# Kernel optimization log

Measured on AMD Instinct MI355X. Metric: run time of the kernel, lower is better.

Reference implementation:

```python
import jax, jax.numpy as jnp
import numpy as np

D = 1024; H = 16; N = 64; F = 4096
B = 1; T = 2048
W_LORA = 64; A_LORA = 64; V_LORA = 32; G_LORA = 128


def rmsnorm(x, w, eps=1e-6):
    x32 = x.astype(jnp.float32)
    var = jnp.mean(x32 * x32, axis=-1, keepdims=True)
    return w * (x32 * jax.lax.rsqrt(var + eps))


def rwkv7_scan(r, w_log, k, v, a, b, state):
    # r,w_log,k,v,a,b: [B,T,H,N]; state: [B,H,N,N] (value dim, key dim)
    decay = jnp.exp(w_log)  # kernel applies exp to the log-decay w = -exp(w_pre)
    def step(S, inp):
        r_t, d_t, k_t, v_t, a_t, b_t = inp  # each [B,H,N]
        sa = jnp.einsum('bhij,bhj->bhi', S, a_t)
        S = S * d_t[:, :, None, :] + sa[..., None] * b_t[:, :, None, :] + v_t[..., None] * k_t[:, :, None, :]
        o_t = jnp.einsum('bhij,bhj->bhi', S, r_t)
        return S, o_t
    seq = tuple(jnp.moveaxis(t, 1, 0) for t in (r, decay, k, v, a, b))  # [T,B,H,N]
    state_f, o = jax.lax.scan(step, state, seq)
    return jnp.moveaxis(o, 0, 1), state_f  # [B,T,H,N], [B,H,N,N]


def setup_inputs() -> dict:
    key = jax.random.key(0)
    ks = iter(jax.random.split(key, 64))
    def nrm(shape, s=1.0):
        return jax.random.normal(next(ks), shape, dtype=jnp.float32) * s
    def uni(shape):
        return jax.random.uniform(next(ks), shape, dtype=jnp.float32)
    WS = 0.02  # weight scale for big matrices
    inp = {
        'x': nrm((B, T, D)),
        'x_prev': nrm((B, D)),
        'v_first': nrm((B, T, D)),
        'state': jnp.zeros((B, H, N, N), jnp.float32),
        'ln1_w': jnp.ones((D,), jnp.float32),
        'ln2_w': jnp.ones((D,), jnp.float32),
        'x_r': uni((1, 1, D)), 'x_w': uni((1, 1, D)), 'x_k': uni((1, 1, D)),
        'x_v': uni((1, 1, D)), 'x_a': uni((1, 1, D)), 'x_g': uni((1, 1, D)),
        'w0': nrm((1, 1, D), 0.5), 'w1': nrm((D, W_LORA), WS), 'w2': nrm((W_LORA, D), WS),
        'a0': nrm((1, 1, D), 0.1), 'a1': nrm((D, A_LORA), WS), 'a2': nrm((A_LORA, D), WS),
        'v0': nrm((1, 1, D), 0.1), 'v1': nrm((D, V_LORA), WS), 'v2': nrm((V_LORA, D), WS),
        'g1': nrm((D, G_LORA), WS), 'g2': nrm((G_LORA, D), WS),
        'k_k': uni((D,)), 'k_a': uni((D,)), 'r_k': nrm((D,), 0.1),
        'R_': nrm((D, D), WS), 'K_': nrm((D, D), WS), 'V_': nrm((D, D), WS), 'O_': nrm((D, D), WS),
        'gate_w': nrm((D, F), WS), 'up_w': nrm((D, F), WS), 'down_w': nrm((F, D), WS),
    }
    return inp


def _block(x, x_prev, v_first, state, ln1_w, ln2_w, x_r, x_w, x_k, x_v, x_a, x_g,
           w0, w1, w2, a0, a1, a2, v0, v1, v2, g1, g2, k_k, k_a, r_k,
           R_, K_, V_, O_, gate_w, up_w, down_w):
    Bx, Tx, _ = x.shape
    xn = rmsnorm(x, ln1_w)  # ln1
    # token shift
    xx = jnp.concatenate([x_prev[:, None, :], xn[:, :-1]], axis=1) - xn
    xr = xn + xx * x_r; xw = xn + xx * x_w; xk = xn + xx * x_k
    xv = xn + xx * x_v; xa = xn + xx * x_a; xg = xn + xx * x_g
    r = xr @ R_
    w_pre = -jax.nn.softplus(-(w0 + jnp.tanh(xw @ w1) @ w2)) - 0.5
    k = xk @ K_
    v = xv @ V_
    a = jax.nn.sigmoid(a0 + (xa @ a1) @ a2)
    g = jax.nn.sigmoid(xg @ g1) @ g2
    kk = (k * k_k).reshape(Bx, Tx, H, N)
    kk = kk / jnp.maximum(jnp.linalg.norm(kk, axis=-1, keepdims=True), 1e-12)
    kk = kk.reshape(Bx, Tx, H * N)
    k = k * (1 + (a - 1) * k_a)
    # layer_id > 0: lerp toward v_first
    v = v + (v_first - v) * jax.nn.sigmoid(v0 + (xv @ v1) @ v2)
    w_log = -jnp.exp(w_pre)  # log-decay passed to the recurrent kernel
    aa = -kk
    bb = kk * a
    hv = lambda t: t.reshape(Bx, Tx, H, N)
    o, state_f = rwkv7_scan(hv(r), hv(w_log), hv(k), hv(v), hv(aa), hv(bb), state)
    o = o.reshape(Bx, Tx, H * N)
    bonus = ((r * k * r_k).reshape(Bx, Tx, H, N).sum(-1, keepdims=True) * v.reshape(Bx, Tx, H, N)).reshape(Bx, Tx, H * N)
    o = o + bonus
    x = x + (o * g) @ O_
    # SwiGLU MLP
    xm = rmsnorm(x, ln2_w)
    x = x + (jax.nn.silu(xm @ gate_w) * (xm @ up_w)) @ down_w
    return x, xn[:, -1], state_f


def reference(x, x_prev, v_first, state, ln1_w, ln2_w, x_r, x_w, x_k, x_v, x_a, x_g,
              w0, w1, w2, a0, a1, a2, v0, v1, v2, g1, g2, k_k, k_a, r_k,
              R_, K_, V_, O_, gate_w, up_w, down_w):
    return _block(x, x_prev, v_first, state, ln1_w, ln2_w, x_r, x_w, x_k, x_v, x_a, x_g,
                  w0, w1, w2, a0, a1, a2, v0, v1, v2, g1, g2, k_k, k_a, r_k,
                  R_, K_, V_, O_, gate_w, up_w, down_w)
```

## Files before the change

kernel.cpp:

```cpp
#include <hip/hip_runtime.h>
#include <math.h>

#define T_ 2048
#define D_ 1024
#define H_ 16
#define N_ 64
#define F_ 4096
#define NCHUNK 64
#define CLEN 32

typedef __attribute__((ext_vector_type(8))) short bf16x8;
typedef __attribute__((ext_vector_type(4))) float f32x4;
typedef __attribute__((address_space(3))) unsigned int lds_u32_t;
typedef __attribute__((address_space(1))) const unsigned int glb_u32_t;

static __device__ __forceinline__ float sigf(float x) { return 1.0f / (1.0f + __expf(-x)); }

static __device__ __forceinline__ ushort f2bf(float f) {
    union { float f; unsigned u; } c; c.f = f;
    unsigned r = (c.u + 0x7FFFu + ((c.u >> 16) & 1u)) >> 16;
    return (ushort)r;
}
static __device__ __forceinline__ float bf2f(ushort h) {
    union { unsigned u; float f; } c; c.u = ((unsigned)h) << 16;
    return c.f;
}

static __device__ __forceinline__ void st4(float* p, float4 v) { *(float4*)p = v; }
static __device__ __forceinline__ void st4(ushort* p, float4 v) {
    ushort4 o; o.x = f2bf(v.x); o.y = f2bf(v.y); o.z = f2bf(v.z); o.w = f2bf(v.w);
    *(ushort4*)p = o;
}

template <typename OutT>
__global__ __launch_bounds__(256) void rmsnorm_kernel(const float* __restrict__ x,
                                                      const float* __restrict__ w,
                                                      OutT* __restrict__ out,
                                                      float* __restrict__ last) {
    const int t = blockIdx.x;
    const int tid = threadIdx.x;
    const float4* xr = (const float4*)(x + (size_t)t * D_);
    float4 v = xr[tid];
    float ss = v.x * v.x + v.y * v.y + v.z * v.z + v.w * v.w;
    ss += __shfl_xor(ss, 1);
    ss += __shfl_xor(ss, 2);
    ss += __shfl_xor(ss, 4);
    ss += __shfl_xor(ss, 8);
    ss += __shfl_xor(ss, 16);
    ss += __shfl_xor(ss, 32);
    __shared__ float red[4];
    if ((tid & 63) == 0) red[tid >> 6] = ss;
    __syncthreads();
    float tot = red[0] + red[1] + red[2] + red[3];
    float scale = rsqrtf(tot * (1.0f / (float)D_) + 1e-6f);
    float4 wv = ((const float4*)w)[tid];
    float4 o;
    o.x = wv.x * v.x * scale;
    o.y = wv.y * v.y * scale;
    o.z = wv.z * v.z * scale;
    o.w = wv.w * v.w * scale;
    st4(out + (size_t)t * D_ + tid * 4, o);
    if (last != nullptr && t == T_ - 1) ((float4*)last)[tid] = o;
}

__global__ __launch_bounds__(256) void rmsnorm_reduce2(
    const float* __restrict__ x, const float* __restrict__ p0, const float* __restrict__ p1,
    const float* __restrict__ w, float* __restrict__ resid_out, ushort* __restrict__ xm) {
    const int t = blockIdx.x;
    const int tid = threadIdx.x;
    const size_t base = (size_t)t * D_ + tid * 4;
    float4 v = *(const float4*)(x + base);
    float4 a = *(const float4*)(p0 + base);
    float4 b = *(const float4*)(p1 + base);
    v.x += a.x + b.x; v.y += a.y + b.y; v.z += a.z + b.z; v.w += a.w + b.w;
    st4(resid_out + base, v);
    float ss = v.x * v.x + v.y * v.y + v.z * v.z + v.w * v.w;
    ss += __shfl_xor(ss, 1);
    ss += __shfl_xor(ss, 2);
    ss += __shfl_xor(ss, 4);
    ss += __shfl_xor(ss, 8);
    ss += __shfl_xor(ss, 16);
    ss += __shfl_xor(ss, 32);
    __shared__ float red[4];
    if ((tid & 63) == 0) red[tid >> 6] = ss;
    __syncthreads();
    float tot = red[0] + red[1] + red[2] + red[3];
    float scale = rsqrtf(tot * (1.0f / (float)D_) + 1e-6f);
    float4 wv = ((const float4*)w)[tid];
    float4 o;
    o.x = wv.x * v.x * scale;
    o.y = wv.y * v.y * scale;
    o.z = wv.z * v.z * scale;
    o.w = wv.w * v.w * scale;
    st4(xm + base, o);
}

__global__ __launch_bounds__(256) void add4_kernel(float* __restrict__ out,
                                                   const float* __restrict__ p,
                                                   int n4slice) {
    const int i = blockIdx.x * 256 + threadIdx.x;
    const float4* p4 = (const float4*)p;
    float4 o = ((const float4*)out)[i];
    float4 a = p4[i], b = p4[i + n4slice], c = p4[i + 2 * n4slice], d = p4[i + 3 * n4slice];
    o.x += (a.x + b.x) + (c.x + d.x);
    o.y += (a.y + b.y) + (c.y + d.y);
    o.z += (a.z + b.z) + (c.z + d.z);
    o.w += (a.w + b.w) + (c.w + d.w);
    ((float4*)out)[i] = o;
}

__global__ __launch_bounds__(256) void shift_kernel(
    const float* __restrict__ xn, const float* __restrict__ x_prev,
    const float* __restrict__ cr, const float* __restrict__ cw, const float* __restrict__ ck,
    const float* __restrict__ cv, const float* __restrict__ ca, const float* __restrict__ cg,
    ushort* __restrict__ xr, ushort* __restrict__ xw, ushort* __restrict__ xk,
    ushort* __restrict__ xv, ushort* __restrict__ xa, ushort* __restrict__ xg) {
    const int i = blockIdx.x * 256 + threadIdx.x;
    const int t = i >> 8, j = i & 255;
    const float4* xn4 = (const float4*)xn;
    float4 cur = xn4[i];
    float4 prev = (t == 0) ? ((const float4*)x_prev)[j] : xn4[i - 256];
    float4 xx;
    xx.x = prev.x - cur.x;
    xx.y = prev.y - cur.y;
    xx.z = prev.z - cur.z;
    xx.w = prev.w - cur.w;
#define APPLY(dst, c)                                   \
    {                                                   \
        float4 cc = ((const float4*)c)[j];              \
        float4 o;                                       \
        o.x = cur.x + xx.x * cc.x;                      \
        o.y = cur.y + xx.y * cc.y;                      \
        o.z = cur.z + xx.z * cc.z;                      \
        o.w = cur.w + xx.w * cc.w;                      \
        st4(dst + (size_t)i * 4, o);                    \
    }
    APPLY(xr, cr)
    APPLY(xw, cw)
    APPLY(xk, ck)
    APPLY(xv, cv)
    APPLY(xa, ca)
    APPLY(xg, cg)
#undef APPLY
}

struct TDesc { const float* in; ushort* out; int K, N, off; };
struct TPack { TDesc d[15]; };

__global__ __launch_bounds__(256) void transpose_cast_multi(TPack p) {
    __shared__ float tile[32][33];
    const int bid = blockIdx.x;
    int di = 0;
#pragma unroll
    for (int i = 1; i < 15; i++)
        if (bid >= p.d[i].off) di = i;
    const TDesc d = p.d[di];
    const int local = bid - d.off;
    const int nt = d.N >> 5;
    const int bx = local % nt, by = local / nt;
    const int tx = threadIdx.x & 31, ty = threadIdx.x >> 5;
    const int n0 = bx * 32, k0 = by * 32;
#pragma unroll
    for (int i = 0; i < 4; i++)
        tile[ty + i * 8][tx] = d.in[(size_t)(k0 + ty + i * 8) * d.N + n0 + tx];
    __syncthreads();
#pragma unroll
    for (int i = 0; i < 4; i++)
        d.out[(size_t)(n0 + ty + i * 8) * d.K + k0 + tx] = f2bf(tile[tx][ty + i * 8]);
}

template <typename OutT, bool PARTIAL>
__global__ __launch_bounds__(256) void mfma_gemm(
    const ushort* __restrict__ A, const ushort* __restrict__ BT, OutT* __restrict__ C,
    const float* res, int M, int Ntot, int K, int klen, int epi) {
    __shared__ ushort As[2][128 * 32];
    __shared__ ushort Bs[2][128 * 32];
    const int tid = threadIdx.x;
    const int wave = tid >> 6, lane = tid & 63;
    const int wr = wave >> 1, wc = wave & 1;
    const int lrow = lane & 15, quad = lane >> 4;
    int bx = blockIdx.x, by = blockIdx.y;
    if (gridDim.x == 8 && gridDim.y == 16) {
        const int bid = by * 8 + bx;
        const int k = bid & 7, i = bid >> 3;
        bx = ((k & 1) << 2) + (i & 3);
        by = ((k >> 1) << 2) + (i >> 2);
    }
    const int m0 = by * 128, n0 = bx * 128;
    const int kbase = blockIdx.z * klen;
    const int srow = lane >> 2;
    const int scol = (lane & 3) << 3;

    f32x4 acc[4][4] = {};

    auto stage = [&](int buf, int kk) {
#pragma unroll
        for (int j = 0; j < 2; j++) {
            const int chunk = 2 * wave + j;
            const ushort* ga = A + (size_t)(m0 + chunk * 16 + srow) * K + kk + scol;
            __builtin_amdgcn_global_load_lds((glb_u32_t*)ga,
                                             (lds_u32_t*)&As[buf][chunk * 512], 16, 0, 0);
            const int brow = n0 + chunk * 16 + srow;
            if (brow < Ntot) {
                const ushort* gb = BT + (size_t)brow * K + kk + scol;
                __builtin_amdgcn_global_load_lds((glb_u32_t*)gb,
                                                 (lds_u32_t*)&Bs[buf][chunk * 512], 16, 0, 0);
            }
        }
    };

    stage(0, kbase);
    __syncthreads();
    int cur = 0;
    for (int k0 = kbase; k0 < kbase + klen; k0 += 32) {
        if (k0 + 32 < kbase + klen) stage(cur ^ 1, k0 + 32);
        bf16x8 af[4], bfr[4];
#pragma unroll
        for (int mi = 0; mi < 4; mi++)
            af[mi] = *(const bf16x8*)&As[cur][(wr * 64 + mi * 16 + lrow) * 32 + quad * 8];
#pragma unroll
        for (int ni = 0; ni < 4; ni++)
            bfr[ni] = *(const bf16x8*)&Bs[cur][(wc * 64 + ni * 16 + lrow) * 32 + quad * 8];
#pragma unroll
        for (int mi = 0; mi < 4; mi++)
#pragma unroll
            for (int ni = 0; ni < 4; ni++)
                acc[mi][ni] = __builtin_amdgcn_mfma_f32_16x16x32_bf16(af[mi], bfr[ni], acc[mi][ni], 0, 0, 0);
        __syncthreads();
        cur ^= 1;
    }

    const size_t zoff = PARTIAL ? (size_t)blockIdx.z * M * Ntot : 0;
#pragma unroll
    for (int mi = 0; mi < 4; mi++) {
#pragma unroll
        for (int r = 0; r < 4; r++) {
            const int row = m0 + wr * 64 + mi * 16 + quad * 4 + r;
#pragma unroll
            for (int ni = 0; ni < 4; ni++) {
                const int col = n0 + wc * 64 + ni * 16 + lrow;
                if (col < Ntot) {
                    const size_t idx = (size_t)row * Ntot + col;
                    float val = acc[mi][ni][r];
                    if constexpr (PARTIAL) {
                        ((float*)C)[idx + zoff] = val;
                    } else {
                        if (epi == 1) val += res[idx];
                        if constexpr (sizeof(OutT) == 2) C[idx] = (OutT)f2bf(val);
                        else C[idx] = (OutT)val;
                    }
                }
            }
        }
    }
}

struct MMDesc {
    const ushort* A; const ushort* BT;
    float* Cf; ushort* Cb;
    const float* res; const float* res2; const float* bias;
    int Ntot, K, epi;
};
template <int NZ>
struct MMPack { MMDesc d[NZ]; };

template <int NZ>
__global__ __launch_bounds__(256) void mfma_gemm_multi(MMPack<NZ> p) {
    const MMDesc d = p.d[blockIdx.z];
    const int n0 = blockIdx.x * 128;
    if (n0 >= d.Ntot) return;
    __shared__ ushort As[2][128 * 32];
    __shared__ ushort Bs[2][128 * 32];
    const int tid = threadIdx.x;
    const int wave = tid >> 6, lane = tid & 63;
    const int wr = wave >> 1, wc = wave & 1;
    const int lrow = lane & 15, quad = lane >> 4;
    const int m0 = blockIdx.y * 128;
    const int srow = lane >> 2;
    const int scol = (lane & 3) << 3;
    const int K = d.K, Ntot = d.Ntot;

    f32x4 acc[4][4] = {};

    auto stage = [&](int buf, int kk) {
#pragma unroll
        for (int j = 0; j < 2; j++) {
            const int chunk = 2 * wave + j;
            const ushort* ga = d.A + (size_t)(m0 + chunk * 16 + srow) * K + kk + scol;
            __builtin_amdgcn_global_load_lds((glb_u32_t*)ga,
                                             (lds_u32_t*)&As[buf][chunk * 512], 16, 0, 0);
            const int brow = n0 + chunk * 16 + srow;
            if (brow < Ntot) {
                const ushort* gb = d.BT + (size_t)brow * K + kk + scol;
                __builtin_amdgcn_global_load_lds((glb_u32_t*)gb,
                                                 (lds_u32_t*)&Bs[buf][chunk * 512], 16, 0, 0);
            }
        }
    };

    stage(0, 0);
    __syncthreads();
    int cur = 0;
    for (int k0 = 0; k0 < K; k0 += 32) {
        if (k0 + 32 < K) stage(cur ^ 1, k0 + 32);
        bf16x8 af[4], bfr[4];
#pragma unroll
        for (int mi = 0; mi < 4; mi++)
            af[mi] = *(const bf16x8*)&As[cur][(wr * 64 + mi * 16 + lrow) * 32 + quad * 8];
#pragma unroll
        for (int ni = 0; ni < 4; ni++)
            bfr[ni] = *(const bf16x8*)&Bs[cur][(wc * 64 + ni * 16 + lrow) * 32 + quad * 8];
#pragma unroll
        for (int mi = 0; mi < 4; mi++)
#pragma unroll
            for (int ni = 0; ni < 4; ni++)
                acc[mi][ni] = __builtin_amdgcn_mfma_f32_16x16x32_bf16(af[mi], bfr[ni], acc[mi][ni], 0, 0, 0);
        __syncthreads();
        cur ^= 1;
    }

#pragma unroll
    for (int mi = 0; mi < 4; mi++) {
#pragma unroll
        for (int r = 0; r < 4; r++) {
            const int row = m0 + wr * 64 + mi * 16 + quad * 4 + r;
#pragma unroll
            for (int ni = 0; ni < 4; ni++) {
                const int col = n0 + wc * 64 + ni * 16 + lrow;
                if (col < Ntot) {
                    const size_t idx = (size_t)row * Ntot + col;
                    float val = acc[mi][ni][r];
                    switch (d.epi) {
                        case 3: val = tanhf(val); break;
                        case 4: val = sigf(val); break;
                        case 5: val = sigf(d.bias[col] + val); break;
                        case 6: val = __expf(-0.60653065971263342f * sigf(d.bias[col] + val)); break;
                        case 7: {
                            float vr = d.res[idx];
                            val = vr + (d.res2[idx] - vr) * sigf(d.bias[col] + val);
                        } break;
                        default: break;
                    }
                    if (d.Cb) d.Cb[idx] = f2bf(val);
                    else d.Cf[idx] = val;
                }
            }
        }
    }
}

__global__ __launch_bounds__(256) void kk_kernel(float* __restrict__ k,
                                                 const float* __restrict__ a_sig,
                                                 const float* __restrict__ k_k,
                                                 const float* __restrict__ k_a,
                                                 float* __restrict__ kk,
                                                 float* __restrict__ mb) {
    const int b = blockIdx.x * 4 + (threadIdx.x >> 6);
    const int t = b >> 4, h = b & 15;
    const int lane = threadIdx.x & 63;
    const size_t idx = (size_t)t * D_ + h * N_ + lane;
    const int wi = h * N_ + lane;
    const float kraw = k[idx];
    const float kv = kraw * k_k[wi];
    float ss = kv * kv;
    ss += __shfl_xor(ss, 1);
    ss += __shfl_xor(ss, 2);
    ss += __shfl_xor(ss, 4);
    ss += __shfl_xor(ss, 8);
    ss += __shfl_xor(ss, 16);
    ss += __shfl_xor(ss, 32);
    const float nrm = fmaxf(sqrtf(ss), 1e-12f);
    const float kkn = kv / nrm;
    kk[idx] = kkn;
    mb[idx] = -kkn * a_sig[idx];
    k[idx] = kraw * (1.0f + (a_sig[idx] - 1.0f) * k_a[wi]);
}

#define FOR16(M) M(0) M(1) M(2) M(3) M(4) M(5) M(6) M(7) \
                 M(8) M(9) M(10) M(11) M(12) M(13) M(14) M(15)

__global__ __launch_bounds__(64, 1) void scan_pass1(
    const float* __restrict__ gR, const float* __restrict__ gD, const float* __restrict__ gK,
    const float* __restrict__ gV, const float* __restrict__ gKK, const float* __restrict__ gMB,
    float* __restrict__ Pbuf, float* __restrict__ Lbuf,
    float* __restrict__ zbuf, float* __restrict__ olbuf) {
    const int bid = blockIdx.x;
    const int h = bid & 15;
    const int c = bid >> 4;
    const int lane = threadIdx.x;
    const int hb = h * N_;
    const int t0 = c * CLEN;
    const int tend = t0 + CLEN - 1;

    __shared__ __align__(16) unsigned char ring[2 * 2048];

    const int rsel = lane >> 4;
    const int sub4 = (lane & 15) << 2;
    const float* p1 = (rsel == 0 ? gR : rsel == 1 ? gD : rsel == 2 ? gK : gKK)
                      + (size_t)t0 * D_ + hb + sub4;
    const float* p2 = (rsel == 1 ? gV : gMB) + (size_t)t0 * D_ + hb + sub4;

#define DECLP(q) f32x4 sp##q = {(lane == 4 * q + 0) ? 1.0f : 0.0f, \
                                (lane == 4 * q + 1) ? 1.0f : 0.0f, \
                                (lane == 4 * q + 2) ? 1.0f : 0.0f, \
                                (lane == 4 * q + 3) ? 1.0f : 0.0f};
    FOR16(DECLP)
#undef DECLP
#define DECLL(q) f32x4 sl##q = {0.f, 0.f, 0.f, 0.f};
    FOR16(DECLL)
#undef DECLL

    float4 r0a, r0b, r1a, r1b, r2a, r2b, r3a, r3b;

#define LOADQ(qa, qb, tt) {                                                  \
        const size_t _adv = (size_t)((tt) - t0) * D_;                        \
        qa = *(const float4*)(p1 + _adv);                                    \
        qb = *(const float4*)(p2 + _adv); }
#define WRITEQ(sl, qa, qb) {                                                 \
        *(float4*)(ring + (sl) * 2048 + lane * 16) = qa;                     \
        *(float4*)(ring + (sl) * 2048 + 1024 + lane * 16) = qb; }
#define PA(q) { const f32x4 kk4 = sKKr[q];                                   \
        pacc += sp##q * kk4; lacc += sl##q * kk4; }
#define PB(q) {                                                   \
        const f32x4 d4 = sDr[q];                                  \
        const f32x4 k4 = sKr[q];                                  \
        const f32x4 m4 = sMBr[q];                                 \
        const f32x4 r4 = sRr[q];                                  \
        sp##q = sp##q * d4 + m4 * sapP;                           \
        sl##q = sl##q * d4 + (m4 * sapL + k4 * vv);               \
        oP += sp##q * r4;                                         \
        oL += sl##q * r4;                                         \
    }
#define COMPUTE(sl, tt) {                                                    \
        const unsigned char* sb = (const unsigned char*)ring + (sl) * 2048;  \
        const f32x4* sRr = (const f32x4*)(sb);                               \
        const f32x4* sDr = (const f32x4*)(sb + 256);                         \
        const f32x4* sKr = (const f32x4*)(sb + 512);                         \
        const f32x4* sKKr = (const f32x4*)(sb + 768);                        \
        const f32x4* sMBr = (const f32x4*)(sb + 1024);                       \
        const float* sVr = (const float*)(sb + 1280);                        \
        f32x4 pacc = {0.f, 0.f, 0.f, 0.f};                                   \
        f32x4 lacc = {0.f, 0.f, 0.f, 0.f};                                   \
        FOR16(PA)                                                            \
        const float sapP = (pacc.x + pacc.y) + (pacc.z + pacc.w);            \
        const float sapL = (lacc.x + lacc.y) + (lacc.z + lacc.w);            \
        const float vv = sVr[lane];                                          \
        f32x4 oP = {0.f, 0.f, 0.f, 0.f};                                     \
        f32x4 oL = {0.f, 0.f, 0.f, 0.f};                                     \
        FOR16(PB)                                                            \
        zbuf[(size_t)(tt) * D_ + hb + lane] = (oP.x + oP.y) + (oP.z + oP.w); \
        olbuf[(size_t)(tt) * D_ + hb + lane] = (oL.x + oL.y) + (oL.z + oL.w); }

    LOADQ(r0a, r0b, t0)
    LOADQ(r1a, r1b, t0 + 1)
    LOADQ(r2a, r2b, t0 + 2)
    LOADQ(r3a, r3b, t0 + 3)
    WRITEQ(0, r0a, r0b)

    for (int t = t0; t < t0 + CLEN; t += 4) {
        WRITEQ(1, r1a, r1b)
        LOADQ(r0a, r0b, (t + 4 > tend ? tend : t + 4))
        COMPUTE(0, t)
        WRITEQ(0, r2a, r2b)
        LOADQ(r1a, r1b, (t + 5 > tend ? tend : t + 5))
        COMPUTE(1, t + 1)
        WRITEQ(1, r3a, r3b)
        LOADQ(r2a, r2b, (t + 6 > tend ? tend : t + 6))
        COMPUTE(0, t + 2)
        WRITEQ(0, r0a, r0b)
        LOADQ(r3a, r3b, (t + 7 > tend ? tend : t + 7))
        COMPUTE(1, t + 3)
    }
#undef COMPUTE
#undef PB
#undef PA
#undef WRITEQ
#undef LOADQ

    const size_t base = ((size_t)c * 16 + h) * 4096 + (size_t)lane * 64;
#define STP(q) *(f32x4*)(Pbuf + base + 4 * q) = sp##q;
    FOR16(STP)
#undef STP
#define STL(q) *(f32x4*)(Lbuf + base + 4 * q) = sl##q;
    FOR16(STL)
#undef STL
}

__global__ __launch_bounds__(256) void scan_combine(
    const float* __restrict__ state_in, const float* __restrict__ Pbuf,
    const float* __restrict__ Lbuf, float* __restrict__ SstT, float* __restrict__ state_out) {
    const int h = blockIdx.x >> 2, rg = blockIdx.x & 3;
    const int tid = threadIdx.x;
    const int i = tid >> 4, j4 = (tid & 15) << 2;
    const int gi = rg * 16 + i;
    __shared__ float Sl[16][68];
    __shared__ float Pl[64][68];

    float4 sv = *(const float4*)(state_in + (size_t)h * 4096 + gi * 64 + j4);
    *(float4*)&Sl[i][j4] = sv;
    __syncthreads();

    for (int c = 0; c < NCHUNK; c++) {
        const size_t cb = ((size_t)c * 16 + h) * 4096;
        float4 scur = *(const float4*)&Sl[i][j4];
        SstT[cb + (size_t)(j4 + 0) * 64 + gi] = scur.x;
        SstT[cb + (size_t)(j4 + 1) * 64 + gi] = scur.y;
        SstT[cb + (size_t)(j4 + 2) * 64 + gi] = scur.z;
        SstT[cb + (size_t)(j4 + 3) * 64 + gi] = scur.w;
#pragma unroll
        for (int q = 0; q < 4; q++) {
            const int pr = (tid >> 4) + q * 16;
            *(float4*)&Pl[pr][j4] = *(const float4*)(Pbuf + cb + (size_t)pr * 64 + j4);
        }
        __syncthreads();
        float4 acc = *(const float4*)(Lbuf + cb + (size_t)gi * 64 + j4);
#pragma unroll 8
        for (int m = 0; m < 64; m++) {
            const float smv = Sl[i][m];
            const float4 p4 = *(const float4*)&Pl[m][j4];
            acc.x = fmaf(smv, p4.x, acc.x);
            acc.y = fmaf(smv, p4.y, acc.y);
            acc.z = fmaf(smv, p4.z, acc.z);
            acc.w = fmaf(smv, p4.w, acc.w);
        }
        __syncthreads();
        *(float4*)&Sl[i][j4] = acc;
        __syncthreads();
    }
    *(float4*)(state_out + (size_t)h * 4096 + gi * 64 + j4) = *(const float4*)&Sl[i][j4];
}

__global__ __launch_bounds__(256) void scan_fix(
    const float* __restrict__ zbuf, const float* __restrict__ olbuf,
    const float* __restrict__ SstT, float* __restrict__ o) {
    const int tg = blockIdx.x >> 4, h = blockIdx.x & 15;
    const int hb = h * N_;
    const int tid = threadIdx.x;
    const int tok = tid >> 4, i4 = (tid & 15) << 2;
    const int tbase = tg * 16;
    const int c = tbase / CLEN;
    __shared__ float zl[16][68];
    __shared__ float Sl[64][68];

    *(float4*)&zl[tok][i4] = *(const float4*)(zbuf + (size_t)(tbase + tok) * D_ + hb + i4);
    const size_t cb = ((size_t)c * 16 + h) * 4096;
#pragma unroll
    for (int q = 0; q < 4; q++) {
        const int jr = (tid >> 4) + q * 16;
        *(float4*)&Sl[jr][i4] = *(const float4*)(SstT + cb + (size_t)jr * 64 + i4);
    }
    __syncthreads();
    float4 acc = *(const float4*)(olbuf + (size_t)(tbase + tok) * D_ + hb + i4);
#pragma unroll 8
    for (int j = 0; j < 64; j++) {
        const float zv = zl[tok][j];
        const float4 p4 = *(const float4*)&Sl[j][i4];
        acc.x = fmaf(zv, p4.x, acc.x);
        acc.y = fmaf(zv, p4.y, acc.y);
        acc.z = fmaf(zv, p4.z, acc.z);
        acc.w = fmaf(zv, p4.w, acc.w);
    }
    *(float4*)(o + (size_t)(tbase + tok) * D_ + hb + i4) = acc;
}

__global__ __launch_bounds__(256) void bonus_kernel(const float* __restrict__ o,
                                                    const float* __restrict__ r,
                                                    const float* __restrict__ k,
                                                    const float* __restrict__ v,
                                                    const float* __restrict__ g,
                                                    const float* __restrict__ r_k,
                                                    ushort* __restrict__ og) {
    const int b = blockIdx.x * 4 + (threadIdx.x >> 6);
    const int t = b >> 4, h = b & 15;
    const int lane = threadIdx.x & 63;
    const size_t idx = (size_t)t * D_ + h * N_ + lane;
    float c = r[idx] * k[idx] * r_k[h * N_ + lane];
    c += __shfl_xor(c, 1);
    c += __shfl_xor(c, 2);
    c += __shfl_xor(c, 4);
    c += __shfl_xor(c, 8);
    c += __shfl_xor(c, 16);
    c += __shfl_xor(c, 32);
    const float on = o[idx] + c * v[idx];
    og[idx] = f2bf(on * g[idx]);
}

__global__ __launch_bounds__(256) void mulz_kernel(const ushort* __restrict__ Z,
                                                   ushort* __restrict__ Hb) {
    const int idx = blockIdx.x * 256 + threadIdx.x;
    const int t = idx >> 10;
    const int j = (idx & 1023) << 2;
    const ushort4 zg = *(const ushort4*)(Z + (size_t)t * 8192 + j);
    const ushort4 zu = *(const ushort4*)(Z + (size_t)t * 8192 + 4096 + j);
    ushort4 o;
    float g0 = bf2f(zg.x), g1 = bf2f(zg.y), g2 = bf2f(zg.z), g3 = bf2f(zg.w);
    o.x = f2bf(g0 * sigf(g0) * bf2f(zu.x));
    o.y = f2bf(g1 * sigf(g1) * bf2f(zu.y));
    o.z = f2bf(g2 * sigf(g2) * bf2f(zu.z));
    o.w = f2bf(g3 * sigf(g3) * bf2f(zu.w));
    *(ushort4*)(Hb + (size_t)t * 4096 + j) = o;
}

extern "C" void kernel_launch(void* const* d_in, const int* in_sizes, int n_in,
                              void* d_out, int out_size, void* d_ws, size_t ws_size,
                              hipStream_t stream) {
    const float* x      = (const float*)d_in[0];
    const float* x_prev = (const float*)d_in[1];
    const float* v_first= (const float*)d_in[2];
    const float* state  = (const float*)d_in[3];
    const float* ln1_w  = (const float*)d_in[4];
    const float* ln2_w  = (const float*)d_in[5];
    const float* x_r    = (const float*)d_in[6];
    const float* x_w    = (const float*)d_in[7];
    const float* x_k    = (const float*)d_in[8];
    const float* x_v    = (const float*)d_in[9];
    const float* x_a    = (const float*)d_in[10];
    const float* x_g    = (const float*)d_in[11];
    const float* w0     = (const float*)d_in[12];
    const float* w1     = (const float*)d_in[13];
    const float* w2     = (const float*)d_in[14];
    const float* a0     = (const float*)d_in[15];
    const float* a1     = (const float*)d_in[16];
    const float* a2     = (const float*)d_in[17];
    const float* v0     = (const float*)d_in[18];
    const float* v1     = (const float*)d_in[19];
    const float* v2     = (const float*)d_in[20];
    const float* g1     = (const float*)d_in[21];
    const float* g2     = (const float*)d_in[22];
    const float* k_k    = (const float*)d_in[23];
    const float* k_a    = (const float*)d_in[24];
    const float* r_k    = (const float*)d_in[25];
    const float* R_     = (const float*)d_in[26];
    const float* K_     = (const float*)d_in[27];
    const float* V_     = (const float*)d_in[28];
    const float* O_     = (const float*)d_in[29];
    const float* gate_w = (const float*)d_in[30];
    const float* up_w   = (const float*)d_in[31];
    const float* down_w = (const float*)d_in[32];

    float* ws = (float*)d_ws;
    const size_t U = (size_t)T_ * D_;
    float* u_r  = ws;
    float* u_k  = ws + 1 * U;
    float* u_v  = ws + 2 * U;
    float* u_dc = ws + 3 * U;
    float* u_kk = ws + 4 * U;
    float* u_mb = ws + 5 * U;
    float* u_g  = ws + 6 * U;
    float* u_ao = ws + 7 * U;
    ushort* XB = (ushort*)(ws + 8 * U);
    const size_t TD = U;
    ushort* XR = XB + 0 * TD;
    ushort* XW = XB + 1 * TD;
    ushort* XK = XB + 2 * TD;
    ushort* XV = XB + 3 * TD;
    ushort* XA = XB + 4 * TD;
    ushort* XG = XB + 5 * TD;
    float* Pbuf  = (float*)XB;
    float* Lbuf  = u_g;
    float* zbuf  = ws + 10 * U;
    float* olbuf = (float*)d_out;
    float* SstT  = u_dc;
    float* obuf  = u_mb;
    ushort* OG   = XB;
    ushort* XM   = (ushort*)(ws + 10 * U);
    float* Opart = ws + 4 * U;
    ushort* Zbuf = (ushort*)ws;
    ushort* Hbuf = (ushort*)(ws + 4 * U);
    float* Dpart = ws;
    ushort* WT = (ushort*)(ws + 11 * U);
    const size_t DD = (size_t)D_ * D_;
    const size_t DF = (size_t)D_ * F_;
    ushort* WTR = WT;
    ushort* WTK = WTR + DD;
    ushort* WTV = WTK + DD;
    ushort* WTO = WTV + DD;
    ushort* WTG = WTO + DD;
    ushort* WTU = WTG + DF;
    ushort* WTD = WTU + DF;
    ushort* WTw1 = WTD + DF;
    ushort* WTw2 = WTw1 + 64 * 1024;
    ushort* WTa1 = WTw2 + 64 * 1024;
    ushort* WTa2 = WTa1 + 64 * 1024;
    ushort* WTv1 = WTa2 + 64 * 1024;
    ushort* WTv2 = WTv1 + 32 * 1024;
    ushort* WTg1 = WTv2 + 32 * 1024;
    ushort* WTg2 = WTg1 + 128 * 1024;
    ushort* Lw = WTg2 + 128 * 1024;
    ushort* La = Lw + (size_t)T_ * 64;
    ushort* Lv = La + (size_t)T_ * 64;
    ushort* Lg = Lv + (size_t)T_ * 32;

    float* out_x = (float*)d_out;
    float* out_xn_last = out_x + (size_t)T_ * D_;
    float* out_state = out_xn_last + D_;

    TPack tp;
    int toff = 0, ti = 0;
    auto addT = [&](const float* in, ushort* out, int K, int N) {
        tp.d[ti].in = in; tp.d[ti].out = out; tp.d[ti].K = K; tp.d[ti].N = N; tp.d[ti].off = toff;
        toff += (N / 32) * (K / 32); ++ti;
    };
    addT(R_, WTR, D_, D_);
    addT(K_, WTK, D_, D_);
    addT(V_, WTV, D_, D_);
    addT(O_, WTO, D_, D_);
    addT(gate_w, WTG, D_, F_);
    addT(up_w, WTU, D_, F_);
    addT(down_w, WTD, F_, D_);
    addT(w1, WTw1, D_, 64);
    addT(w2, WTw2, 64, D_);
    addT(a1, WTa1, D_, 64);
    addT(a2, WTa2, 64, D_);
    addT(v1, WTv1, D_, 32);
    addT(v2, WTv2, 32, D_);
    addT(g1, WTg1, D_, 128);
    addT(g2, WTg2, 128, D_);
    transpose_cast_multi<<<toff, 256, 0, stream>>>(tp);

    rmsnorm_kernel<float><<<T_, 256, 0, stream>>>(x, ln1_w, out_x, out_xn_last);
    shift_kernel<<<T_, 256, 0, stream>>>(out_x, x_prev, x_r, x_w, x_k, x_v, x_a, x_g,
                                         XR, XW, XK, XV, XA, XG);
    auto mkmm = [](const ushort* A, const ushort* BT, float* Cf, ushort* Cb,
                   const float* res, const float* res2, const float* bias,
                   int Ntot, int K, int epi) {
        MMDesc m{A, BT, Cf, Cb, res, res2, bias, Ntot, K, epi};
        return m;
    };
    MMPack<7> pa;
    pa.d[0] = mkmm(XR, WTR, u_r, nullptr, nullptr, nullptr, nullptr, D_, D_, 0);
    pa.d[1] = mkmm(XK, WTK, u_k, nullptr, nullptr, nullptr, nullptr, D_, D_, 0);
    pa.d[2] = mkmm(XV, WTV, u_v, nullptr, nullptr, nullptr, nullptr, D_, D_, 0);
    pa.d[3] = mkmm(XW, WTw1, nullptr, Lw, nullptr, nullptr, nullptr, 64,  D_, 3);
    pa.d[4] = mkmm(XA, WTa1, nullptr, La, nullptr, nullptr, nullptr, 64,  D_, 0);
    pa.d[5] = mkmm(XV, WTv1, nullptr, Lv, nullptr, nullptr, nullptr, 32,  D_, 0);
    pa.d[6] = mkmm(XG, WTg1, nullptr, Lg, nullptr, nullptr, nullptr, 128, D_, 4);
    mfma_gemm_multi<7><<<dim3(8, 16, 7), 256, 0, stream>>>(pa);
    MMPack<3> pb;
    pb.d[0] = mkmm(Lw, WTw2, u_dc, nullptr, nullptr, nullptr, w0, D_, 64,  6);
    pb.d[1] = mkmm(La, WTa2, u_ao, nullptr, nullptr, nullptr, a0, D_, 64,  5);
    pb.d[2] = mkmm(Lv, WTv2, u_v,  nullptr, u_v, v_first,     v0, D_, 32,  7);
    mfma_gemm_multi<3><<<dim3(8, 16, 3), 256, 0, stream>>>(pb);
    kk_kernel<<<T_ * H_ / 4, 256, 0, stream>>>(u_k, u_ao, k_k, k_a, u_kk, u_mb);
    scan_pass1<<<NCHUNK * H_, 64, 0, stream>>>(u_r, u_dc, u_k, u_v, u_kk, u_mb,
                                               Pbuf, Lbuf, zbuf, olbuf);
    scan_combine<<<H_ * 4, 256, 0, stream>>>(state, Pbuf, Lbuf, SstT, out_state);
    mfma_gemm<float, false><<<dim3(8, 16), 256, 0, stream>>>(
        Lg, WTg2, u_g, nullptr, T_, D_, 128, 128, 0);
    scan_fix<<<(T_ / 16) * H_, 256, 0, stream>>>(zbuf, olbuf, SstT, obuf);
    bonus_kernel<<<T_ * H_ / 4, 256, 0, stream>>>(obuf, u_r, u_k, u_v, u_g, r_k, OG);
    mfma_gemm<float, true><<<dim3(8, 16, 2), 256, 0, stream>>>(
        OG, WTO, Opart, nullptr, T_, D_, D_, 512, 0);
    rmsnorm_reduce2<<<T_, 256, 0, stream>>>(x, Opart, Opart + U, ln2_w, out_x, XM);
    mfma_gemm<ushort, false><<<dim3(64, 16), 256, 0, stream>>>(
        XM, WTG, Zbuf, nullptr, T_, 2 * F_, D_, D_, 0);
    mulz_kernel<<<(T_ * (F_ / 4)) / 256, 256, 0, stream>>>(Zbuf, Hbuf);
    mfma_gemm<float, true><<<dim3(8, 16, 4), 256, 0, stream>>>(
        Hbuf, WTD, Dpart, nullptr, T_, D_, F_, 1024, 0);
    add4_kernel<<<(int)(U / 4 / 256), 256, 0, stream>>>(out_x, Dpart, (int)(U / 4));
}
```

Baseline: 647.8 us.

## Halve serial chunk-state combine via parallel pairwise merge and odd-chunk fill

```diff
diff --git a/kernel.cpp b/kernel.cpp
--- a/kernel.cpp
+++ b/kernel.cpp
@@ -486,6 +486,68 @@
 #undef STL
 }
 
+__global__ __launch_bounds__(64) void merge_pairs(float* __restrict__ Pbuf,
+                                                  float* __restrict__ Lbuf) {
+    const int h = blockIdx.x & 15, j = blockIdx.x >> 4;
+    const int t = threadIdx.x;
+    __shared__ float PaT[64][65];
+    __shared__ float LaT[64][65];
+    __shared__ float Pb[64][68];
+    const size_t ca = ((size_t)(2 * j) * 16 + h) * 4096;
+    const size_t cb = ((size_t)(2 * j + 1) * 16 + h) * 4096;
+#pragma unroll
+    for (int q = 0; q < 16; q++) {
+        const int idx = t + q * 64;
+        const int r = idx >> 4, c4 = (idx & 15) << 2;
+        float4 pa = *(const float4*)(Pbuf + ca + (size_t)r * 64 + c4);
+        float4 la = *(const float4*)(Lbuf + ca + (size_t)r * 64 + c4);
+        float4 pb = *(const float4*)(Pbuf + cb + (size_t)r * 64 + c4);
+        PaT[c4 + 0][r] = pa.x; PaT[c4 + 1][r] = pa.y;
+        PaT[c4 + 2][r] = pa.z; PaT[c4 + 3][r] = pa.w;
+        LaT[c4 + 0][r] = la.x; LaT[c4 + 1][r] = la.y;
+        LaT[c4 + 2][r] = la.z; LaT[c4 + 3][r] = la.w;
+        *(float4*)&Pb[r][c4] = pb;
+    }
+    __syncthreads();
+    const int cg = (t & 3) << 4;
+    const int r0 = (t >> 2) << 2;
+    float4 accP[4][4] = {};
+    float4 accL[4][4];
+#pragma unroll
+    for (int rr = 0; rr < 4; rr++)
+#pragma unroll
+        for (int e = 0; e < 4; e++)
+            accL[rr][e] = *(const float4*)(Lbuf + cb + (size_t)(r0 + rr) * 64 + cg + 4 * e);
+    for (int m = 0; m < 64; m++) {
+        float4 pb4[4];
+#pragma unroll
+        for (int e = 0; e < 4; e++) pb4[e] = *(const float4*)&Pb[m][cg + 4 * e];
+#pragma unroll
+        for (int rr = 0; rr < 4; rr++) {
+            const float pa = PaT[m][r0 + rr];
+            const float la = LaT[m][r0 + rr];
+#pragma unroll
+            for (int e = 0; e < 4; e++) {
+                accP[rr][e].x = fmaf(pa, pb4[e].x, accP[rr][e].x);
+                accP[rr][e].y = fmaf(pa, pb4[e].y, accP[rr][e].y);
+                accP[rr][e].z = fmaf(pa, pb4[e].z, accP[rr][e].z);
+                accP[rr][e].w = fmaf(pa, pb4[e].w, accP[rr][e].w);
+                accL[rr][e].x = fmaf(la, pb4[e].x, accL[rr][e].x);
+                accL[rr][e].y = fmaf(la, pb4[e].y, accL[rr][e].y);
+                accL[rr][e].z = fmaf(la, pb4[e].z, accL[rr][e].z);
+                accL[rr][e].w = fmaf(la, pb4[e].w, accL[rr][e].w);
+            }
+        }
+    }
+#pragma unroll
+    for (int rr = 0; rr < 4; rr++)
+#pragma unroll
+        for (int e = 0; e < 4; e++) {
+            *(float4*)(Pbuf + cb + (size_t)(r0 + rr) * 64 + cg + 4 * e) = accP[rr][e];
+            *(float4*)(Lbuf + cb + (size_t)(r0 + rr) * 64 + cg + 4 * e) = accL[rr][e];
+        }
+}
+
 __global__ __launch_bounds__(256) void scan_combine(
     const float* __restrict__ state_in, const float* __restrict__ Pbuf,
     const float* __restrict__ Lbuf, float* __restrict__ SstT, float* __restrict__ state_out) {
@@ -498,22 +560,39 @@
 
     float4 sv = *(const float4*)(state_in + (size_t)h * 4096 + gi * 64 + j4);
     *(float4*)&Sl[i][j4] = sv;
+
+    float4 rp0, rp1, rp2, rp3, rl;
+    {
+        const size_t cb = ((size_t)1 * 16 + h) * 4096;
+        rp0 = *(const float4*)(Pbuf + cb + (size_t)(i +  0) * 64 + j4);
+        rp1 = *(const float4*)(Pbuf + cb + (size_t)(i + 16) * 64 + j4);
+        rp2 = *(const float4*)(Pbuf + cb + (size_t)(i + 32) * 64 + j4);
+        rp3 = *(const float4*)(Pbuf + cb + (size_t)(i + 48) * 64 + j4);
+        rl  = *(const float4*)(Lbuf + cb + (size_t)gi * 64 + j4);
+    }
     __syncthreads();
 
-    for (int c = 0; c < NCHUNK; c++) {
-        const size_t cb = ((size_t)c * 16 + h) * 4096;
+    for (int c = 0; c < NCHUNK / 2; c++) {
+        *(float4*)&Pl[i +  0][j4] = rp0;
+        *(float4*)&Pl[i + 16][j4] = rp1;
+        *(float4*)&Pl[i + 32][j4] = rp2;
+        *(float4*)&Pl[i + 48][j4] = rp3;
+        float4 acc = rl;
+        const size_t so = ((size_t)(2 * c) * 16 + h) * 4096;
         float4 scur = *(const float4*)&Sl[i][j4];
-        SstT[cb + (size_t)(j4 + 0) * 64 + gi] = scur.x;
-        SstT[cb + (size_t)(j4 + 1) * 64 + gi] = scur.y;
-        SstT[cb + (size_t)(j4 + 2) * 64 + gi] = scur.z;
-        SstT[cb + (size_t)(j4 + 3) * 64 + gi] = scur.w;
-#pragma unroll
-        for (int q = 0; q < 4; q++) {
-            const int pr = (tid >> 4) + q * 16;
-            *(float4*)&Pl[pr][j4] = *(const float4*)(Pbuf + cb + (size_t)pr * 64 + j4);
+        SstT[so + (size_t)(j4 + 0) * 64 + gi] = scur.x;
+        SstT[so + (size_t)(j4 + 1) * 64 + gi] = scur.y;
+        SstT[so + (size_t)(j4 + 2) * 64 + gi] = scur.z;
+        SstT[so + (size_t)(j4 + 3) * 64 + gi] = scur.w;
+        __syncthreads();
+        if (c + 1 < NCHUNK / 2) {
+            const size_t cb = ((size_t)(2 * c + 3) * 16 + h) * 4096;
+            rp0 = *(const float4*)(Pbuf + cb + (size_t)(i +  0) * 64 + j4);
+            rp1 = *(const float4*)(Pbuf + cb + (size_t)(i + 16) * 64 + j4);
+            rp2 = *(const float4*)(Pbuf + cb + (size_t)(i + 32) * 64 + j4);
+            rp3 = *(const float4*)(Pbuf + cb + (size_t)(i + 48) * 64 + j4);
+            rl  = *(const float4*)(Lbuf + cb + (size_t)gi * 64 + j4);
         }
-        __syncthreads();
-        float4 acc = *(const float4*)(Lbuf + cb + (size_t)gi * 64 + j4);
 #pragma unroll 8
         for (int m = 0; m < 64; m++) {
             const float smv = Sl[i][m];
@@ -525,9 +604,50 @@
         }
         __syncthreads();
         *(float4*)&Sl[i][j4] = acc;
-        __syncthreads();
     }
     *(float4*)(state_out + (size_t)h * 4096 + gi * 64 + j4) = *(const float4*)&Sl[i][j4];
+}
+
+__global__ __launch_bounds__(256) void scan_oddfill(
+    const float* __restrict__ Pbuf, const float* __restrict__ Lbuf,
+    float* __restrict__ SstT) {
+    const int b = blockIdx.x;
+    const int rg = b & 3, h = (b >> 2) & 15, j = b >> 6;
+    const int tid = threadIdx.x;
+    const int i = tid >> 4, j4 = (tid & 15) << 2;
+    const int gi = rg * 16 + i;
+    __shared__ float Sl[16][68];
+    __shared__ float Pl[64][68];
+    const size_t ce = ((size_t)(2 * j) * 16 + h) * 4096;
+    const size_t co = ((size_t)(2 * j + 1) * 16 + h) * 4096;
+    {
+        float4 s;
+        s.x = SstT[ce + (size_t)(j4 + 0) * 64 + gi];
+        s.y = SstT[ce + (size_t)(j4 + 1) * 64 + gi];
+        s.z = SstT[ce + (size_t)(j4 + 2) * 64 + gi];
+        s.w = SstT[ce + (size_t)(j4 + 3) * 64 + gi];
+        *(float4*)&Sl[i][j4] = s;
+    }
+#pragma unroll
+    for (int q = 0; q < 4; q++) {
+        const int prq = i + q * 16;
+        *(float4*)&Pl[prq][j4] = *(const float4*)(Pbuf + ce + (size_t)prq * 64 + j4);
+    }
+    __syncthreads();
+    float4 acc = *(const float4*)(Lbuf + ce + (size_t)gi * 64 + j4);
+#pragma unroll 8
+    for (int m = 0; m < 64; m++) {
+        const float smv = Sl[i][m];
+        const float4 p4 = *(const float4*)&Pl[m][j4];
+        acc.x = fmaf(smv, p4.x, acc.x);
+        acc.y = fmaf(smv, p4.y, acc.y);
+        acc.z = fmaf(smv, p4.z, acc.z);
+        acc.w = fmaf(smv, p4.w, acc.w);
+    }
+    SstT[co + (size_t)(j4 + 0) * 64 + gi] = acc.x;
+    SstT[co + (size_t)(j4 + 1) * 64 + gi] = acc.y;
+    SstT[co + (size_t)(j4 + 2) * 64 + gi] = acc.z;
+    SstT[co + (size_t)(j4 + 3) * 64 + gi] = acc.w;
 }
 
 __global__ __launch_bounds__(256) void scan_fix(
@@ -744,7 +864,9 @@
     kk_kernel<<<T_ * H_ / 4, 256, 0, stream>>>(u_k, u_ao, k_k, k_a, u_kk, u_mb);
     scan_pass1<<<NCHUNK * H_, 64, 0, stream>>>(u_r, u_dc, u_k, u_v, u_kk, u_mb,
                                                Pbuf, Lbuf, zbuf, olbuf);
+    merge_pairs<<<16 * 32, 64, 0, stream>>>(Pbuf, Lbuf);
     scan_combine<<<H_ * 4, 256, 0, stream>>>(state, Pbuf, Lbuf, SstT, out_state);
+    scan_oddfill<<<16 * 32 * 4, 256, 0, stream>>>(Pbuf, Lbuf, SstT);
     mfma_gemm<float, false><<<dim3(8, 16), 256, 0, stream>>>(
         Lg, WTg2, u_g, nullptr, T_, D_, 128, 128, 0);
     scan_fix<<<(T_ / 16) * H_, 256, 0, stream>>>(zbuf, olbuf, SstT, obuf);
```

Measured after the change: 620.1 us. 4.3% less time.
